# Optimization experiments

Measured on AMD Instinct MI355X. Metric: run time of the kernel, lower is better.

Reference implementation:

```python
import jax, jax.numpy as jnp
import numpy as np
import math

EPS = 1e-5
GROUPS = 32

def group_norm(x, gamma, beta, groups=GROUPS, eps=EPS):
    B, C, H, W = x.shape
    xr = x.reshape(B, groups, C // groups, H, W)
    m = xr.mean(axis=(2, 3, 4), keepdims=True)
    v = xr.var(axis=(2, 3, 4), keepdims=True)
    xr = (xr - m) * jax.lax.rsqrt(v + eps)
    x = xr.reshape(B, C, H, W)
    return x * gamma[None, :, None, None] + beta[None, :, None, None]

def swish(x):
    return x * jax.nn.sigmoid(x)

def conv2d(x, w, b=None, padding='SAME'):
    # x: NCHW, w: OIHW
    y = jax.lax.conv_general_dilated(x, w, window_strides=(1, 1), padding=padding,
                                     dimension_numbers=('NCHW', 'OIHW', 'NCHW'))
    if b is not None:
        y = y + b[None, :, None, None]
    return y

def setup_inputs() -> dict:
    key = jax.random.key(0)
    ks = jax.random.split(key, 24)
    B, C, H, W = 16, 256, 32, 32
    NE = 256  # noise_level_emb_dim
    s = 0.02
    inp = {
        'x': jax.random.normal(ks[0], (B, C, H, W), jnp.float32),
        'time_emb': jax.random.normal(ks[1], (B, NE), jnp.float32),
        'c': jax.random.normal(ks[2], (B, C, H, W), jnp.float32),
        # block1: GroupNorm + Swish + Conv3x3(dim -> dim_out)
        'gn1_g': jnp.ones((C,), jnp.float32),
        'gn1_b': jnp.zeros((C,), jnp.float32),
        'conv1_w': jax.random.normal(ks[3], (C, C, 3, 3), jnp.float32) * s,
        'conv1_b': jnp.zeros((C,), jnp.float32),
        # FeatureWiseAffine linear (use_affine_level=False): Linear(NE -> dim_out)
        'noise_w': jax.random.normal(ks[4], (C, NE), jnp.float32) * s,
        'noise_b': jnp.zeros((C,), jnp.float32),
        # block2: GroupNorm + Swish + Conv3x3(dim_out -> dim_out)
        'gn2_g': jnp.ones((C,), jnp.float32),
        'gn2_b': jnp.zeros((C,), jnp.float32),
        'conv2_w': jax.random.normal(ks[5], (C, C, 3, 3), jnp.float32) * s,
        'conv2_b': jnp.zeros((C,), jnp.float32),
        # c_func: Conv1x1(dim_out -> dim_out)
        'cfunc_w': jax.random.normal(ks[6], (C, C, 1, 1), jnp.float32) * s,
        'cfunc_b': jnp.zeros((C,), jnp.float32),
        # attention: GroupNorm, qkv Conv1x1 (no bias), out Conv1x1
        'attn_gn_g': jnp.ones((C,), jnp.float32),
        'attn_gn_b': jnp.zeros((C,), jnp.float32),
        'qkv_w': jax.random.normal(ks[7], (3 * C, C, 1, 1), jnp.float32) * s,
        'out_w': jax.random.normal(ks[8], (C, C, 1, 1), jnp.float32) * s,
        'out_b': jnp.zeros((C,), jnp.float32),
    }
    return inp

def reference(x, time_emb, c,
              gn1_g, gn1_b, conv1_w, conv1_b,
              noise_w, noise_b,
              gn2_g, gn2_b, conv2_w, conv2_b,
              cfunc_w, cfunc_b,
              attn_gn_g, attn_gn_b, qkv_w, out_w, out_b):
    B, C, H, W = x.shape
    # ---- ResnetBlock ----
    h = conv2d(swish(group_norm(x, gn1_g, gn1_b)), conv1_w, conv1_b)
    # FeatureWiseAffine (additive): h + Linear(time_emb) broadcast over HxW
    h = h + (time_emb @ noise_w.T + noise_b)[:, :, None, None]
    h = conv2d(swish(group_norm(h, gn2_g, gn2_b)), conv2_w, conv2_b)
    h = conv2d(c, cfunc_w, cfunc_b) + h
    h = h + x  # res_conv is Identity since dim == dim_out
    # ---- SelfAttention (n_head=1) ----
    n = group_norm(h, attn_gn_g, attn_gn_b)
    qkv = conv2d(n, qkv_w)                       # [B, 3C, H, W]
    q, k, v = jnp.split(qkv.reshape(B, 3 * C, H * W), 3, axis=1)  # each [B, C, HW]
    scores = jnp.einsum('bcs,bct->bst', q, k) / math.sqrt(C)      # [B, HW, HW]
    attn = jax.nn.softmax(scores, axis=-1)
    o = jnp.einsum('bst,bct->bcs', attn, v).reshape(B, C, H, W)
    o = conv2d(o, out_w, out_b)
    return o + h
```

## Files before the change

### kernel.cpp

```cpp
#include <hip/hip_runtime.h>
#include <hip/hip_bf16.h>
#include <math.h>

typedef __hip_bfloat16 bf16;
typedef short short8 __attribute__((ext_vector_type(8)));
typedef float floatx4 __attribute__((ext_vector_type(4)));

#define NB 16
#define NC 256
#define NHW 1024
#define NNE 256
#define NP (NB*NC*NHW)

__device__ __forceinline__ unsigned short f2bu(float f){
  bf16 h = (bf16)f; return *(unsigned short*)&h;
}

template<bool SWISH>
__global__ void gn_t_kernel(const float* __restrict__ src, const float* __restrict__ gamma,
                            const float* __restrict__ beta, short* __restrict__ xp){
  int b = blockIdx.x >> 5, g = blockIdx.x & 31;
  const int GSZ = 8*NHW;
  size_t base = ((size_t)b*NC + g*8)*NHW;
  int tid = threadIdx.x;
  float s = 0.f, ss = 0.f;
  for (int i = tid; i < GSZ; i += 256){
    float v = src[base+i];
    s += v; ss += v*v;
  }
  __shared__ float rs[256], rq[256];
  rs[tid] = s; rq[tid] = ss;
  __syncthreads();
  for (int off=128; off>0; off>>=1){
    if (tid < off){ rs[tid]+=rs[tid+off]; rq[tid]+=rq[tid+off]; }
    __syncthreads();
  }
  float mean = rs[0] * (1.f/GSZ);
  float var  = rq[0] * (1.f/GSZ) - mean*mean;
  float inv  = rsqrtf(var + 1e-5f);
  float gm[8], bt[8];
  #pragma unroll
  for (int j=0;j<8;j++){ gm[j] = gamma[g*8+j]*inv; bt[j] = beta[g*8+j]; }
  short* dst = xp + (((size_t)b*8 + (g>>2))*NHW)*32 + (g&3)*8;
  for (int px = tid; px < NHW; px += 256){
    short8 pk;
    #pragma unroll
    for (int j=0;j<8;j++){
      float v = (src[base + j*NHW + px] - mean)*gm[j] + bt[j];
      if (SWISH) v = v / (1.f + __expf(-v));
      pk[j] = (short)f2bu(v);
    }
    *(short8*)(dst + (size_t)px*32) = pk;
  }
}

template<bool SWISH>
__global__ void gn_post_kernel(const float* __restrict__ src, const float* __restrict__ st,
                               const float* __restrict__ gamma, const float* __restrict__ beta,
                               short* __restrict__ xp){
  int b = blockIdx.x >> 5, g = blockIdx.x & 31;
  size_t base = ((size_t)b*NC + g*8)*NHW;
  int tid = threadIdx.x;
  float s  = st[(b*32+g)*2+0];
  float ss = st[(b*32+g)*2+1];
  float mean = s * (1.f/8192.f);
  float var  = ss * (1.f/8192.f) - mean*mean;
  float inv  = rsqrtf(var + 1e-5f);
  float gm[8], bt[8];
  #pragma unroll
  for (int j=0;j<8;j++){ gm[j] = gamma[g*8+j]*inv; bt[j] = beta[g*8+j]; }
  short* dst = xp + (((size_t)b*8 + (g>>2))*NHW)*32 + (g&3)*8;
  for (int px = tid; px < NHW; px += 256){
    short8 pk;
    #pragma unroll
    for (int j=0;j<8;j++){
      float v = (src[base + j*NHW + px] - mean)*gm[j] + bt[j];
      if (SWISH) v = v / (1.f + __expf(-v));
      pk[j] = (short)f2bu(v);
    }
    *(short8*)(dst + (size_t)px*32) = pk;
  }
}

__global__ void wprep3_kernel(const float* __restrict__ w1, const float* __restrict__ w2,
                              short* __restrict__ wp1, short* __restrict__ wp2,
                              float* __restrict__ st){
  int co = blockIdx.x & 255;
  const float* w = (blockIdx.x < 256) ? w1 : w2;
  short* wp = (blockIdx.x < 256) ? wp1 : wp2;
  int tid = threadIdx.x;
  if (blockIdx.x == 0){
    for (int i=tid;i<2048;i+=256) st[i] = 0.f;
  }
  __shared__ float tmp[2304];
  for (int i=tid;i<2304;i+=256) tmp[i] = w[(size_t)co*2304 + i];
  __syncthreads();
  for (int j=tid;j<2304;j+=256){
    int tap = j>>8, ci = j&255;
    wp[(((size_t)tap*8 + (ci>>5))*NC + co)*32 + (ci&31)] = (short)f2bu(tmp[ci*9 + tap]);
  }
}

__global__ void wprep1_kernel(const float* __restrict__ wq, const float* __restrict__ wc,
                              const float* __restrict__ wo,
                              short* __restrict__ wqp, short* __restrict__ wcp,
                              short* __restrict__ wop){
  int blk = blockIdx.x, tid = threadIdx.x;
  if (blk < 768){
    float v = wq[(size_t)blk*256 + tid];
    wqp[(((size_t)(tid>>5))*768 + blk)*32 + (tid&31)] = (short)f2bu(v);
  } else if (blk < 1024){
    int co = blk - 768;
    float v = wc[(size_t)co*256 + tid];
    wcp[(((size_t)(tid>>5))*256 + co)*32 + (tid&31)] = (short)f2bu(v);
  } else {
    int co = blk - 1024;
    float v = wo[(size_t)co*256 + tid];
    wop[(((size_t)(tid>>5))*256 + co)*32 + (tid&31)] = (short)f2bu(v);
  }
}

__global__ void cvtc_kernel(const float* __restrict__ c_in, short* __restrict__ cp){
  int pxc = blockIdx.x, cc = blockIdx.y, b = blockIdx.z, tid = threadIdx.x;
  __shared__ float ld[32][257];
  size_t gbase = ((size_t)b*NC + cc*32)*NHW + pxc*256;
  for (int j=0;j<32;j++) ld[j][tid] = c_in[gbase + (size_t)j*NHW + tid];
  __syncthreads();
  short* dst = cp + (((size_t)b*8 + cc)*NHW + pxc*256)*32;
  for (int it=0;it<4;it++){
    int pxl = it*64 + (tid>>2), ckl = tid&3;
    short8 pk;
    #pragma unroll
    for (int e=0;e<8;e++) pk[e] = (short)f2bu(ld[ckl*8+e][pxl]);
    *(short8*)(dst + (size_t)pxl*32 + ckl*8) = pk;
  }
}

__global__ void noise_kernel(const float* __restrict__ emb, const float* __restrict__ w,
                             const float* __restrict__ bias, float* __restrict__ na){
  int b = blockIdx.x, c = threadIdx.x;
  __shared__ float e[NNE];
  e[c] = emb[b*NNE + c];
  __syncthreads();
  float acc = bias[c];
  for (int k=0;k<NNE;k++) acc += e[k]*w[c*NNE+k];
  na[b*NC + c] = acc;
}

#define XSTR 264
__global__ __launch_bounds__(256,1)
void conv3_mfma_kernel(const short* __restrict__ xp, const short* __restrict__ wp,
                       const float* __restrict__ bias, const float* __restrict__ bias_bc,
                       const float* __restrict__ addf, float* __restrict__ out,
                       float* __restrict__ st){
  const int b = blockIdx.y, y0 = blockIdx.x*2;
  const int tid = threadIdx.x, wave = tid>>6, lane = tid&63;
  const int quad = lane>>4, lm = lane&15;
  __shared__ short Xs[4*34*XSTR];

  {
    int r = tid>>6, side = (tid>>5)&1, ck = tid&31;
    short8 z = {0,0,0,0,0,0,0,0};
    *(short8*)&Xs[((r*34) + side*33)*XSTR + ck*8] = z;
  }
  for (int it=0; it<16; ++it){
    int idx = it*256 + tid;
    int r = idx>>10, rem = idx&1023;
    int cc = rem>>7, x = (rem>>2)&31, ckl = rem&3;
    int y = y0 - 1 + r;
    short8 v = {0,0,0,0,0,0,0,0};
    if ((unsigned)y < 32u)
      v = *(const short8*)(xp + (((size_t)b*8 + cc)*NHW + y*32 + x)*32 + ckl*8);
    *(short8*)&Xs[(r*34 + x + 1)*XSTR + (cc*4 + ckl)*8] = v;
  }
  __syncthreads();

  floatx4 acc[4][4];
  #pragma unroll
  for (int mt=0;mt<4;mt++)
    #pragma unroll
    for (int nt=0;nt<4;nt++) acc[mt][nt] = (floatx4){0.f,0.f,0.f,0.f};

  const int co_w = wave*64;
  const int aoff = (co_w + lm)*32 + quad*8;

  auto ldA = [&](int j, short8 a[4]){
    const short* p = wp + (size_t)j*NC*32 + aoff;
    #pragma unroll
    for (int mt=0;mt<4;mt++) a[mt] = *(const short8*)(p + mt*(16*32));
  };
  auto ldB = [&](int j, short8 bf[4]){
    int tap = j>>3, kk = j&7;
    int dy = (tap*11)>>5;
    int dxp = tap - dy*3;
    int base = (lm+dxp)*XSTR + quad*8 + kk*32 + dy*(34*XSTR);
    #pragma unroll
    for (int nt=0;nt<4;nt++)
      bf[nt] = *(const short8*)&Xs[base + (nt>>1)*(34*XSTR) + (nt&1)*(16*XSTR)];
  };

  short8 A[4][4], Bf[4][4];
  ldA(0,A[0]); ldB(0,Bf[0]);
  ldA(1,A[1]); ldB(1,Bf[1]);
  ldA(2,A[2]); ldB(2,Bf[2]);
  ldA(3,A[3]); ldB(3,Bf[3]);
  for (int it=0; it<72; it+=4){
    #pragma unroll
    for (int u=0;u<4;u++){
      #pragma unroll
      for (int mt=0;mt<4;mt++)
        #pragma unroll
        for (int nt=0;nt<4;nt++)
          acc[mt][nt] = __builtin_amdgcn_mfma_f32_16x16x32_bf16(A[u][mt], Bf[u][nt], acc[mt][nt], 0,0,0);
      int j = it + 4 + u; if (j > 71) j = 71;
      ldA(j, A[u]); ldB(j, Bf[u]);
    }
  }

  const int hw0 = blockIdx.x*64;
  float gs[4], gq[4];
  #pragma unroll
  for (int mt=0;mt<4;mt++){ gs[mt]=0.f; gq[mt]=0.f; }
  #pragma unroll
  for (int mt=0;mt<4;mt++){
    #pragma unroll
    for (int r=0;r<4;r++){
      int co = co_w + mt*16 + quad*4 + r;
      float bb = bias[co] + (bias_bc ? bias_bc[b*NC + co] : 0.f);
      size_t ob = ((size_t)b*NC + co)*NHW + hw0;
      #pragma unroll
      for (int nt=0;nt<4;nt++){
        size_t oi = ob + nt*16 + lm;
        float v = acc[mt][nt][r] + bb;
        if (addf) v += addf[oi];
        out[oi] = v;
        gs[mt] += v; gq[mt] += v*v;
      }
    }
  }
  #pragma unroll
  for (int mt=0;mt<4;mt++){
    float s = gs[mt], q = gq[mt];
    #pragma unroll
    for (int o=1;o<32;o<<=1){ s += __shfl_xor(s, o, 64); q += __shfl_xor(q, o, 64); }
    if ((lane&31) == 0){
      int g = (co_w>>3) + mt*2 + (quad>>1);
      atomicAdd(&st[(b*32+g)*2+0], s);
      atomicAdd(&st[(b*32+g)*2+1], q);
    }
  }
}

__global__ __launch_bounds__(256)
void gemm_cfunc_kernel(const short* __restrict__ cp, const short* __restrict__ wcp,
                       const float* __restrict__ bias, const float* __restrict__ xres,
                       float* __restrict__ out){
  const int b = blockIdx.z;
  const int tid = threadIdx.x, wave = tid>>6, lane = tid&63;
  const int quad = lane>>4, lm = lane&15;
  const int M0 = blockIdx.y*128 + (wave>>1)*64;
  const int N0 = blockIdx.x*128 + (wave&1)*64;
  floatx4 acc[4][4];
  #pragma unroll
  for (int mt=0;mt<4;mt++)
    #pragma unroll
    for (int nt=0;nt<4;nt++) acc[mt][nt] = (floatx4){0.f,0.f,0.f,0.f};
  #pragma unroll
  for (int kk=0;kk<8;kk++){
    short8 af[4], bfr[4];
    #pragma unroll
    for (int mt=0;mt<4;mt++)
      af[mt] = *(const short8*)(wcp + ((size_t)kk*256 + M0 + mt*16 + lm)*32 + quad*8);
    #pragma unroll
    for (int nt=0;nt<4;nt++)
      bfr[nt] = *(const short8*)(cp + (((size_t)b*8 + kk)*NHW + N0 + nt*16 + lm)*32 + quad*8);
    #pragma unroll
    for (int mt=0;mt<4;mt++)
      #pragma unroll
      for (int nt=0;nt<4;nt++)
        acc[mt][nt] = __builtin_amdgcn_mfma_f32_16x16x32_bf16(af[mt], bfr[nt], acc[mt][nt], 0,0,0);
  }
  #pragma unroll
  for (int mt=0;mt<4;mt++){
    #pragma unroll
    for (int r=0;r<4;r++){
      int co = M0 + mt*16 + quad*4 + r;
      float bb = bias[co];
      size_t ob = ((size_t)b*NC + co)*NHW + N0;
      #pragma unroll
      for (int nt=0;nt<4;nt++){
        size_t oi = ob + nt*16 + lm;
        out[oi] = acc[mt][nt][r] + bb + xres[oi];
      }
    }
  }
}

__global__ __launch_bounds__(256)
void gemm_qkv_kernel(const short* __restrict__ ntp, const short* __restrict__ wqp,
                     short* __restrict__ qp, short* __restrict__ kp, short* __restrict__ vp){
  const int b = blockIdx.z;
  const int tid = threadIdx.x, wave = tid>>6, lane = tid&63;
  const int quad = lane>>4, lm = lane&15;
  const int M0 = blockIdx.y*128 + (wave>>1)*64;
  const int N0 = blockIdx.x*128 + (wave&1)*64;
  floatx4 acc[4][4];
  #pragma unroll
  for (int mt=0;mt<4;mt++)
    #pragma unroll
    for (int nt=0;nt<4;nt++) acc[mt][nt] = (floatx4){0.f,0.f,0.f,0.f};
  #pragma unroll
  for (int kk=0;kk<8;kk++){
    short8 af[4], bfr[4];
    #pragma unroll
    for (int mt=0;mt<4;mt++)
      af[mt] = *(const short8*)(wqp + ((size_t)kk*768 + M0 + mt*16 + lm)*32 + quad*8);
    #pragma unroll
    for (int nt=0;nt<4;nt++)
      bfr[nt] = *(const short8*)(ntp + (((size_t)b*8 + kk)*NHW + N0 + nt*16 + lm)*32 + quad*8);
    #pragma unroll
    for (int mt=0;mt<4;mt++)
      #pragma unroll
      for (int nt=0;nt<4;nt++)
        acc[mt][nt] = __builtin_amdgcn_mfma_f32_16x16x32_bf16(af[mt], bfr[nt], acc[mt][nt], 0,0,0);
  }
  #pragma unroll
  for (int mt=0;mt<4;mt++){
    int co_base = M0 + mt*16 + quad*4;
    int sec = co_base >> 8;
    int c = co_base & 255;
    #pragma unroll
    for (int nt=0;nt<4;nt++){
      int s = N0 + nt*16 + lm;
      if (sec < 2){
        unsigned short t0 = f2bu(acc[mt][nt][0]), t1 = f2bu(acc[mt][nt][1]);
        unsigned short t2 = f2bu(acc[mt][nt][2]), t3 = f2bu(acc[mt][nt][3]);
        uint2 w2; w2.x = ((unsigned)t1<<16)|t0; w2.y = ((unsigned)t3<<16)|t2;
        short* dst = (sec==0) ? qp : kp;
        *(uint2*)(dst + (((size_t)b*8 + (c>>5))*NHW + s)*32 + (c&31)) = w2;
      } else {
        #pragma unroll
        for (int r=0;r<4;r++)
          vp[(((size_t)b*32 + (s>>5))*NC + c + r)*32 + (s&31)] = (short)f2bu(acc[mt][nt][r]);
      }
    }
  }
}

__global__ __launch_bounds__(1024)
void attn_mfma_kernel(const short* __restrict__ qp, const short* __restrict__ kp,
                      const short* __restrict__ vp, short* __restrict__ op){
  const int bx = blockIdx.x;
  const int b = bx & 15;
  const int s0 = (bx >> 4) * 64;
  const int tid = threadIdx.x, wave = tid>>6, lane = tid&63;
  const int quad = lane>>4, lm = lane&15;

  __shared__ short P[64*1024];
  __shared__ float red[64][16];
  __shared__ float fred[64];

  floatx4 sc[4][4];
  #pragma unroll
  for (int rt=0;rt<4;rt++)
    #pragma unroll
    for (int ti=0;ti<4;ti++) sc[rt][ti] = (floatx4){0.f,0.f,0.f,0.f};

  const int colb = wave*64;
  #pragma unroll
  for (int h=0;h<8;h++){
    const size_t hb = ((size_t)b*8 + h)*NHW;
    short8 aq[4], kf[4];
    #pragma unroll
    for (int rt=0;rt<4;rt++)
      aq[rt] = *(const short8*)(qp + (hb + s0 + rt*16 + lm)*32 + quad*8);
    #pragma unroll
    for (int ti=0;ti<4;ti++)
      kf[ti] = *(const short8*)(kp + (hb + colb + ti*16 + lm)*32 + quad*8);
    #pragma unroll
    for (int rt=0;rt<4;rt++)
      #pragma unroll
      for (int ti=0;ti<4;ti++)
        sc[rt][ti] = __builtin_amdgcn_mfma_f32_16x16x32_bf16(aq[rt], kf[ti], sc[rt][ti], 0,0,0);
  }

  const float scale = 0.0625f;
  float mx[4][4];
  #pragma unroll
  for (int rt=0;rt<4;rt++)
    #pragma unroll
    for (int r=0;r<4;r++) mx[rt][r] = -1e30f;
  #pragma unroll
  for (int rt=0;rt<4;rt++)
    #pragma unroll
    for (int ti=0;ti<4;ti++)
      #pragma unroll
      for (int r=0;r<4;r++){
        float v = sc[rt][ti][r]*scale;
        sc[rt][ti][r] = v;
        mx[rt][r] = fmaxf(mx[rt][r], v);
      }
  #pragma unroll
  for (int o=1;o<16;o<<=1)
    #pragma unroll
    for (int rt=0;rt<4;rt++)
      #pragma unroll
      for (int r=0;r<4;r++) mx[rt][r] = fmaxf(mx[rt][r], __shfl_xor(mx[rt][r], o, 64));
  if (lm==0){
    #pragma unroll
    for (int rt=0;rt<4;rt++)
      #pragma unroll
      for (int r=0;r<4;r++) red[rt*16 + quad*4 + r][wave] = mx[rt][r];
  }
  __syncthreads();
  {
    float v = red[tid>>4][tid&15];
    #pragma unroll
    for (int o=1;o<16;o<<=1) v = fmaxf(v, __shfl_xor(v, o, 64));
    if ((tid&15)==0) fred[tid>>4] = v;
  }
  __syncthreads();
  float fmr[4][4], sm[4][4];
  #pragma unroll
  for (int rt=0;rt<4;rt++)
    #pragma unroll
    for (int r=0;r<4;r++){ fmr[rt][r] = fred[rt*16 + quad*4 + r]; sm[rt][r] = 0.f; }
  #pragma unroll
  for (int rt=0;rt<4;rt++)
    #pragma unroll
    for (int ti=0;ti<4;ti++)
      #pragma unroll
      for (int r=0;r<4;r++){
        float e = __expf(sc[rt][ti][r] - fmr[rt][r]);
        sc[rt][ti][r] = e;
        sm[rt][r] += e;
      }
  #pragma unroll
  for (int o=1;o<16;o<<=1)
    #pragma unroll
    for (int rt=0;rt<4;rt++)
      #pragma unroll
      for (int r=0;r<4;r++) sm[rt][r] += __shfl_xor(sm[rt][r], o, 64);
  __syncthreads();
  if (lm==0){
    #pragma unroll
    for (int rt=0;rt<4;rt++)
      #pragma unroll
      for (int r=0;r<4;r++) red[rt*16 + quad*4 + r][wave] = sm[rt][r];
  }
  __syncthreads();
  {
    float v = red[tid>>4][tid&15];
    #pragma unroll
    for (int o=1;o<16;o<<=1) v += __shfl_xor(v, o, 64);
    if ((tid&15)==0) fred[tid>>4] = 1.f/v;
  }
  __syncthreads();
  float fir[4][4];
  #pragma unroll
  for (int rt=0;rt<4;rt++)
    #pragma unroll
    for (int r=0;r<4;r++) fir[rt][r] = fred[rt*16 + quad*4 + r];
  #pragma unroll
  for (int rt=0;rt<4;rt++)
    #pragma unroll
    for (int ti=0;ti<4;ti++)
      #pragma unroll
      for (int r=0;r<4;r++){
        int row = rt*16 + quad*4 + r;
        int col = colb + ti*16 + lm;
        int off = row*1024 + ((((col>>3) ^ (row&7))&127)<<3) + (col&7);
        P[off] = (short)f2bu(sc[rt][ti][r]*fir[rt][r]);
      }
  __syncthreads();

  const int cg = wave>>1, sh = wave&1;
  const int ch0 = cg*32;
  floatx4 oacc[2][2];
  #pragma unroll
  for (int mt=0;mt<2;mt++)
    #pragma unroll
    for (int nt=0;nt<2;nt++) oacc[mt][nt] = (floatx4){0.f,0.f,0.f,0.f};

  #pragma unroll
  for (int kk=0;kk<32;kk++){
    short8 pf[2], vf[2];
    #pragma unroll
    for (int mt=0;mt<2;mt++){
      int row = sh*32 + mt*16 + lm;
      int off = row*1024 + ((((kk*4 + quad) ^ (row&7))&127)<<3);
      pf[mt] = *(const short8*)(&P[off]);
    }
    #pragma unroll
    for (int nt=0;nt<2;nt++)
      vf[nt] = *(const short8*)(vp + (((size_t)b*32 + kk)*NC + ch0 + nt*16 + lm)*32 + quad*8);
    #pragma unroll
    for (int mt=0;mt<2;mt++)
      #pragma unroll
      for (int nt=0;nt<2;nt++)
        oacc[mt][nt] = __builtin_amdgcn_mfma_f32_16x16x32_bf16(pf[mt], vf[nt], oacc[mt][nt], 0,0,0);
  }

  #pragma unroll
  for (int nt=0;nt<2;nt++){
    int c = ch0 + nt*16 + lm;
    int cc = c>>5, cl = c&31;
    #pragma unroll
    for (int mt=0;mt<2;mt++)
      #pragma unroll
      for (int r=0;r<4;r++){
        int s = s0 + sh*32 + mt*16 + quad*4 + r;
        op[(((size_t)b*8 + cc)*NHW + s)*32 + cl] = (short)f2bu(oacc[mt][nt][r]);
      }
  }
}

__global__ __launch_bounds__(256)
void outproj_mfma_kernel(const short* __restrict__ op, const short* __restrict__ wop,
                         const float* __restrict__ obias, const float* __restrict__ h,
                         float* __restrict__ out){
  const int b = blockIdx.z;
  const int tid = threadIdx.x, wave = tid>>6, lane = tid&63;
  const int quad = lane>>4, lm = lane&15;
  const int M0 = blockIdx.y*128 + (wave>>1)*64;
  const int N0 = blockIdx.x*128 + (wave&1)*64;
  floatx4 acc[4][4];
  #pragma unroll
  for (int mt=0;mt<4;mt++)
    #pragma unroll
    for (int nt=0;nt<4;nt++) acc[mt][nt] = (floatx4){0.f,0.f,0.f,0.f};
  #pragma unroll
  for (int kk=0;kk<8;kk++){
    short8 af[4], bfr[4];
    #pragma unroll
    for (int mt=0;mt<4;mt++)
      af[mt] = *(const short8*)(wop + ((size_t)kk*256 + M0 + mt*16 + lm)*32 + quad*8);
    #pragma unroll
    for (int nt=0;nt<4;nt++)
      bfr[nt] = *(const short8*)(op + (((size_t)b*8 + kk)*NHW + N0 + nt*16 + lm)*32 + quad*8);
    #pragma unroll
    for (int mt=0;mt<4;mt++)
      #pragma unroll
      for (int nt=0;nt<4;nt++)
        acc[mt][nt] = __builtin_amdgcn_mfma_f32_16x16x32_bf16(af[mt], bfr[nt], acc[mt][nt], 0,0,0);
  }
  #pragma unroll
  for (int mt=0;mt<4;mt++){
    #pragma unroll
    for (int r=0;r<4;r++){
      int co = M0 + mt*16 + quad*4 + r;
      float bb = obias[co];
      size_t ob = ((size_t)b*NC + co)*NHW + N0;
      #pragma unroll
      for (int nt=0;nt<4;nt++){
        size_t oi = ob + nt*16 + lm;
        out[oi] = acc[mt][nt][r] + bb + h[oi];
      }
    }
  }
}

extern "C" void kernel_launch(void* const* d_in, const int* in_sizes, int n_in,
                              void* d_out, int out_size, void* d_ws, size_t ws_size,
                              hipStream_t stream){
  const float* x        = (const float*)d_in[0];
  const float* time_emb = (const float*)d_in[1];
  const float* c_in     = (const float*)d_in[2];
  const float* gn1_g    = (const float*)d_in[3];
  const float* gn1_b    = (const float*)d_in[4];
  const float* conv1_w  = (const float*)d_in[5];
  const float* conv1_b  = (const float*)d_in[6];
  const float* noise_w  = (const float*)d_in[7];
  const float* noise_b  = (const float*)d_in[8];
  const float* gn2_g    = (const float*)d_in[9];
  const float* gn2_b    = (const float*)d_in[10];
  const float* conv2_w  = (const float*)d_in[11];
  const float* conv2_b  = (const float*)d_in[12];
  const float* cfunc_w  = (const float*)d_in[13];
  const float* cfunc_b  = (const float*)d_in[14];
  const float* agn_g    = (const float*)d_in[15];
  const float* agn_b    = (const float*)d_in[16];
  const float* qkv_w    = (const float*)d_in[17];
  const float* out_w    = (const float*)d_in[18];
  const float* out_b    = (const float*)d_in[19];
  float* outp = (float*)d_out;

  float* ws = (float*)d_ws;
  float* buf_h = ws;
  float* buf_t = buf_h + NP;
  short* xpb   = (short*)(buf_t + NP);
  short* qp    = xpb + NP;
  short* kp    = qp + NP;
  short* vp    = kp + NP;
  short* wp1   = vp + NP;
  short* wp2   = wp1 + 589824;
  short* wqp   = wp2 + 589824;
  short* wcp   = wqp + 196608;
  short* wop   = wcp + 65536;
  float* na    = (float*)(wop + 65536);
  float* st    = na + NB*NC;
  float* st2   = st;
  float* st3   = st + 1024;
  short* cp    = (short*)buf_t;
  short* op    = (short*)buf_t;

  wprep3_kernel<<<512, 256, 0, stream>>>(conv1_w, conv2_w, wp1, wp2, st);
  wprep1_kernel<<<1280, 256, 0, stream>>>(qkv_w, cfunc_w, out_w, wqp, wcp, wop);
  cvtc_kernel<<<dim3(4,8,NB), 256, 0, stream>>>(c_in, cp);
  noise_kernel<<<NB, 256, 0, stream>>>(time_emb, noise_w, noise_b, na);
  gn_t_kernel<true><<<NB*32, 256, 0, stream>>>(x, gn1_g, gn1_b, xpb);
  conv3_mfma_kernel<<<dim3(16, NB), 256, 0, stream>>>(xpb, wp1, conv1_b, na, nullptr, buf_h, st2);
  gn_post_kernel<true><<<NB*32, 256, 0, stream>>>(buf_h, st2, gn2_g, gn2_b, xpb);
  gemm_cfunc_kernel<<<dim3(8,2,NB), 256, 0, stream>>>(cp, wcp, cfunc_b, x, buf_h);
  conv3_mfma_kernel<<<dim3(16, NB), 256, 0, stream>>>(xpb, wp2, conv2_b, nullptr, buf_h, buf_h, st3);
  gn_post_kernel<false><<<NB*32, 256, 0, stream>>>(buf_h, st3, agn_g, agn_b, xpb);
  gemm_qkv_kernel<<<dim3(8,6,NB), 256, 0, stream>>>(xpb, wqp, qp, kp, vp);
  attn_mfma_kernel<<<256, 1024, 0, stream>>>(qp, kp, vp, op);
  outproj_mfma_kernel<<<dim3(8,2,NB), 256, 0, stream>>>(op, wop, out_b, buf_h, outp);
}
```

Measured before the change: 357.2 us.

## Split conv3x3 K-loop across two wave halves with LDS reduction

```diff
diff --git a/kernel.cpp b/kernel.cpp
--- a/kernel.cpp
+++ b/kernel.cpp
@@ -148,7 +148,7 @@
 }
 
 #define XSTR 264
-__global__ __launch_bounds__(256,1)
+__global__ __launch_bounds__(512,2)
 void conv3_mfma_kernel(const short* __restrict__ xp, const short* __restrict__ wp,
                        const float* __restrict__ bias, const float* __restrict__ bias_bc,
                        const float* __restrict__ addf, float* __restrict__ out,
@@ -156,22 +156,23 @@
   const int b = blockIdx.y, y0 = blockIdx.x*2;
   const int tid = threadIdx.x, wave = tid>>6, lane = tid&63;
   const int quad = lane>>4, lm = lane&15;
+  const int wslice = wave>>1, half = wave&1;
   __shared__ short Xs[4*34*XSTR];
 
-  {
+  if (tid < 256){
     int r = tid>>6, side = (tid>>5)&1, ck = tid&31;
     short8 z = {0,0,0,0,0,0,0,0};
     *(short8*)&Xs[((r*34) + side*33)*XSTR + ck*8] = z;
   }
-  for (int it=0; it<16; ++it){
-    int idx = it*256 + tid;
+  for (int it=0; it<8; ++it){
+    int idx = it*512 + tid;
     int r = idx>>10, rem = idx&1023;
-    int cc = rem>>7, x = (rem>>2)&31, ckl = rem&3;
+    int x = rem>>5, ch = rem&31;
     int y = y0 - 1 + r;
     short8 v = {0,0,0,0,0,0,0,0};
     if ((unsigned)y < 32u)
-      v = *(const short8*)(xp + (((size_t)b*8 + cc)*NHW + y*32 + x)*32 + ckl*8);
-    *(short8*)&Xs[(r*34 + x + 1)*XSTR + (cc*4 + ckl)*8] = v;
+      v = *(const short8*)(xp + (((size_t)b*8 + (ch>>2))*NHW + y*32 + x)*32 + (ch&3)*8);
+    *(short8*)&Xs[(r*34 + x + 1)*XSTR + ch*8] = v;
   }
   __syncthreads();
 
@@ -181,7 +182,7 @@
     #pragma unroll
     for (int nt=0;nt<4;nt++) acc[mt][nt] = (floatx4){0.f,0.f,0.f,0.f};
 
-  const int co_w = wave*64;
+  const int co_w = wslice*64;
   const int aoff = (co_w + lm)*32 + quad*8;
 
   auto ldA = [&](int j, short8 a[4]){
@@ -199,54 +200,77 @@
       bf[nt] = *(const short8*)&Xs[base + (nt>>1)*(34*XSTR) + (nt&1)*(16*XSTR)];
   };
 
+  const int j0 = half*36, jend = j0 + 35;
   short8 A[4][4], Bf[4][4];
-  ldA(0,A[0]); ldB(0,Bf[0]);
-  ldA(1,A[1]); ldB(1,Bf[1]);
-  ldA(2,A[2]); ldB(2,Bf[2]);
-  ldA(3,A[3]); ldB(3,Bf[3]);
-  for (int it=0; it<72; it+=4){
+  ldA(j0+0,A[0]); ldB(j0+0,Bf[0]);
+  ldA(j0+1,A[1]); ldB(j0+1,Bf[1]);
+  ldA(j0+2,A[2]); ldB(j0+2,Bf[2]);
+  ldA(j0+3,A[3]); ldB(j0+3,Bf[3]);
+  for (int it=j0; it<j0+36; it+=4){
     #pragma unroll
     for (int u=0;u<4;u++){
+      __builtin_amdgcn_s_setprio(1);
       #pragma unroll
       for (int mt=0;mt<4;mt++)
         #pragma unroll
         for (int nt=0;nt<4;nt++)
           acc[mt][nt] = __builtin_amdgcn_mfma_f32_16x16x32_bf16(A[u][mt], Bf[u][nt], acc[mt][nt], 0,0,0);
-      int j = it + 4 + u; if (j > 71) j = 71;
+      __builtin_amdgcn_s_setprio(0);
+      int j = it + 4 + u; if (j > jend) j = jend;
       ldA(j, A[u]); ldB(j, Bf[u]);
     }
   }
 
-  const int hw0 = blockIdx.x*64;
-  float gs[4], gq[4];
-  #pragma unroll
-  for (int mt=0;mt<4;mt++){ gs[mt]=0.f; gq[mt]=0.f; }
-  #pragma unroll
-  for (int mt=0;mt<4;mt++){
-    #pragma unroll
-    for (int r=0;r<4;r++){
-      int co = co_w + mt*16 + quad*4 + r;
-      float bb = bias[co] + (bias_bc ? bias_bc[b*NC + co] : 0.f);
-      size_t ob = ((size_t)b*NC + co)*NHW + hw0;
+  __syncthreads();
+  floatx4* red = (floatx4*)Xs;
+  if (half == 1){
+    #pragma unroll
+    for (int mt=0;mt<4;mt++)
+      #pragma unroll
+      for (int nt=0;nt<4;nt++)
+        red[((wslice*16 + mt*4 + nt)*64) + lane] = acc[mt][nt];
+  }
+  __syncthreads();
+  if (half == 0){
+    #pragma unroll
+    for (int mt=0;mt<4;mt++)
       #pragma unroll
       for (int nt=0;nt<4;nt++){
-        size_t oi = ob + nt*16 + lm;
-        float v = acc[mt][nt][r] + bb;
-        if (addf) v += addf[oi];
-        out[oi] = v;
-        gs[mt] += v; gq[mt] += v*v;
-      }
-    }
-  }
-  #pragma unroll
-  for (int mt=0;mt<4;mt++){
-    float s = gs[mt], q = gq[mt];
-    #pragma unroll
-    for (int o=1;o<32;o<<=1){ s += __shfl_xor(s, o, 64); q += __shfl_xor(q, o, 64); }
-    if ((lane&31) == 0){
-      int g = (co_w>>3) + mt*2 + (quad>>1);
-      atomicAdd(&st[(b*32+g)*2+0], s);
-      atomicAdd(&st[(b*32+g)*2+1], q);
+        floatx4 o = red[((wslice*16 + mt*4 + nt)*64) + lane];
+        acc[mt][nt][0]+=o[0]; acc[mt][nt][1]+=o[1]; acc[mt][nt][2]+=o[2]; acc[mt][nt][3]+=o[3];
+      }
+
+    const int hw0 = blockIdx.x*64;
+    float gs[4], gq[4];
+    #pragma unroll
+    for (int mt=0;mt<4;mt++){ gs[mt]=0.f; gq[mt]=0.f; }
+    #pragma unroll
+    for (int mt=0;mt<4;mt++){
+      #pragma unroll
+      for (int r=0;r<4;r++){
+        int co = co_w + mt*16 + quad*4 + r;
+        float bb = bias[co] + (bias_bc ? bias_bc[b*NC + co] : 0.f);
+        size_t ob = ((size_t)b*NC + co)*NHW + hw0;
+        #pragma unroll
+        for (int nt=0;nt<4;nt++){
+          size_t oi = ob + nt*16 + lm;
+          float v = acc[mt][nt][r] + bb;
+          if (addf) v += addf[oi];
+          out[oi] = v;
+          gs[mt] += v; gq[mt] += v*v;
+        }
+      }
+    }
+    #pragma unroll
+    for (int mt=0;mt<4;mt++){
+      float s = gs[mt], q = gq[mt];
+      #pragma unroll
+      for (int o=1;o<32;o<<=1){ s += __shfl_xor(s, o, 64); q += __shfl_xor(q, o, 64); }
+      if ((lane&31) == 0){
+        int g = (co_w>>3) + mt*2 + (quad>>1);
+        atomicAdd(&st[(b*32+g)*2+0], s);
+        atomicAdd(&st[(b*32+g)*2+1], q);
+      }
     }
   }
 }
@@ -609,10 +633,10 @@
   cvtc_kernel<<<dim3(4,8,NB), 256, 0, stream>>>(c_in, cp);
   noise_kernel<<<NB, 256, 0, stream>>>(time_emb, noise_w, noise_b, na);
   gn_t_kernel<true><<<NB*32, 256, 0, stream>>>(x, gn1_g, gn1_b, xpb);
-  conv3_mfma_kernel<<<dim3(16, NB), 256, 0, stream>>>(xpb, wp1, conv1_b, na, nullptr, buf_h, st2);
+  conv3_mfma_kernel<<<dim3(16, NB), 512, 0, stream>>>(xpb, wp1, conv1_b, na, nullptr, buf_h, st2);
   gn_post_kernel<true><<<NB*32, 256, 0, stream>>>(buf_h, st2, gn2_g, gn2_b, xpb);
   gemm_cfunc_kernel<<<dim3(8,2,NB), 256, 0, stream>>>(cp, wcp, cfunc_b, x, buf_h);
-  conv3_mfma_kernel<<<dim3(16, NB), 256, 0, stream>>>(xpb, wp2, conv2_b, nullptr, buf_h, buf_h, st3);
+  conv3_mfma_kernel<<<dim3(16, NB), 512, 0, stream>>>(xpb, wp2, conv2_b, nullptr, buf_h, buf_h, st3);
   gn_post_kernel<false><<<NB*32, 256, 0, stream>>>(buf_h, st3, agn_g, agn_b, xpb);
   gemm_qkv_kernel<<<dim3(8,6,NB), 256, 0, stream>>>(xpb, wqp, qp, kp, vp);
   attn_mfma_kernel<<<256, 1024, 0, stream>>>(qp, kp, vp, op);
```

Measured after the change: 344.2 us. 3.6% less time.
